# Performance work log

Hardware: AMD Instinct MI355X
Metric: run time of the kernel (lower is better)

The kernel has to match this reference:

```python
import jax, jax.numpy as jnp
import numpy as np

GROUP_SIZE = 64

def _dequant(wq, scale, zero):
    # HQQ groupwise dequant: W = (Wq - zero) * scale, groups along input dim.
    out_dim, in_dim = wq.shape
    g = in_dim // GROUP_SIZE
    w = (wq.astype(jnp.float32).reshape(out_dim, g, GROUP_SIZE) - zero[:, :, None]) * scale[:, :, None]
    return w.reshape(out_dim, in_dim)

def setup_inputs() -> dict:
    key = jax.random.key(0)
    ks = jax.random.split(key, 10)
    T, H, I = 256, 4096, 14336
    G1, G2 = H // GROUP_SIZE, I // GROUP_SIZE  # 64, 224
    x = jax.random.normal(ks[0], (T, H), dtype=jnp.float32)
    w1_q = jax.random.randint(ks[1], (I, H), 0, 16, dtype=jnp.int32)
    w1_scale = jax.random.uniform(ks[2], (I, G1), dtype=jnp.float32) * 0.02
    w1_zero = jax.random.uniform(ks[3], (I, G1), dtype=jnp.float32) * 8.0
    w3_q = jax.random.randint(ks[4], (I, H), 0, 16, dtype=jnp.int32)
    w3_scale = jax.random.uniform(ks[5], (I, G1), dtype=jnp.float32) * 0.02
    w3_zero = jax.random.uniform(ks[6], (I, G1), dtype=jnp.float32) * 8.0
    w2_q = jax.random.randint(ks[7], (H, I), 0, 16, dtype=jnp.int32)
    w2_scale = jax.random.uniform(ks[8], (H, G2), dtype=jnp.float32) * 0.02
    w2_zero = jax.random.uniform(ks[9], (H, G2), dtype=jnp.float32) * 8.0
    return {"x": x, "w1_q": w1_q, "w1_scale": w1_scale, "w1_zero": w1_zero,
            "w3_q": w3_q, "w3_scale": w3_scale, "w3_zero": w3_zero,
            "w2_q": w2_q, "w2_scale": w2_scale, "w2_zero": w2_zero}

def reference(x, w1_q, w1_scale, w1_zero, w3_q, w3_scale, w3_zero, w2_q, w2_scale, w2_zero):
    w1 = _dequant(w1_q, w1_scale, w1_zero)  # [I, H]
    w3 = _dequant(w3_q, w3_scale, w3_zero)  # [I, H]
    w2 = _dequant(w2_q, w2_scale, w2_zero)  # [H, I]
    gate = jax.nn.silu(jnp.einsum('th,ih->ti', x, w1))  # [T, I]
    up = jnp.einsum('th,ih->ti', x, w3)                 # [T, I]
    return jnp.einsum('ti,hi->th', gate * up, w2)       # [T, H]
```

## Files before the change

kernel.cpp:

```cpp
#include <hip/hip_runtime.h>
#include <cstdint>
#include <cstddef>

#define T_DIM 256
#define H_DIM 4096
#define I_DIM 14336

typedef __attribute__((ext_vector_type(8))) short s8v;
typedef __attribute__((ext_vector_type(4))) float f4v;

static constexpr size_t XS_BYTES   = (size_t)T_DIM * H_DIM * 2;
static constexpr size_t ACT_OFF    = XS_BYTES;
static constexpr size_t ACT_BYTES  = (size_t)T_DIM * I_DIM * 2;
static constexpr size_t PART_OFF   = ACT_OFF + ACT_BYTES;
static constexpr size_t PART_BYTES = 8ull * T_DIM * H_DIM * 4;
static constexpr size_t WS_NEEDED  = PART_OFF + PART_BYTES;

__device__ __forceinline__ unsigned short f2bf(float f) {
    unsigned u = __builtin_bit_cast(unsigned, f);
    u += 0x7fffu + ((u >> 16) & 1u);
    return (unsigned short)(u >> 16);
}

__device__ __forceinline__ void g2lds16(const void* g, void* l) {
    __builtin_amdgcn_global_load_lds(
        (const __attribute__((address_space(1))) unsigned int*)g,
        (__attribute__((address_space(3))) unsigned int*)l,
        16, 0, 0);
}

__device__ __forceinline__ s8v dq8(const int4 qa, const int4 qb, float s, float ns) {
    union { unsigned short u[8]; s8v v; } r;
    r.u[0] = f2bf(fmaf((float)qa.x, s, ns));
    r.u[1] = f2bf(fmaf((float)qa.y, s, ns));
    r.u[2] = f2bf(fmaf((float)qa.z, s, ns));
    r.u[3] = f2bf(fmaf((float)qa.w, s, ns));
    r.u[4] = f2bf(fmaf((float)qb.x, s, ns));
    r.u[5] = f2bf(fmaf((float)qb.y, s, ns));
    r.u[6] = f2bf(fmaf((float)qb.z, s, ns));
    r.u[7] = f2bf(fmaf((float)qb.w, s, ns));
    return r.v;
}

__global__ __launch_bounds__(256) void k_prep(const float* __restrict__ x,
                                              unsigned short* __restrict__ xs) {
    int gs   = blockIdx.x * 256 + threadIdx.x;
    int kt   = gs >> 11;
    int rem  = gs & 2047;
    int row  = rem >> 3;
    int slot = rem & 7;
    const float* xp = x + (size_t)row * H_DIM + kt * 64 + slot * 8;
    float4 a = *(const float4*)xp;
    float4 b = *(const float4*)(xp + 4);
    union { unsigned short u[8]; s8v v; } r;
    r.u[0] = f2bf(a.x); r.u[1] = f2bf(a.y); r.u[2] = f2bf(a.z); r.u[3] = f2bf(a.w);
    r.u[4] = f2bf(b.x); r.u[5] = f2bf(b.y); r.u[6] = f2bf(b.z); r.u[7] = f2bf(b.w);
    size_t di = (size_t)kt * 16384 + (size_t)row * 64 + (size_t)((slot ^ (row & 7)) * 8);
    *(s8v*)(xs + di) = r.v;
}

__global__ __launch_bounds__(512, 2) void k_gemm1(
    const int* __restrict__ w1q, const float* __restrict__ w1s, const float* __restrict__ w1z,
    const int* __restrict__ w3q, const float* __restrict__ w3s, const float* __restrict__ w3z,
    const unsigned short* __restrict__ xs, unsigned short* __restrict__ act)
{
    __shared__ unsigned char lds[49152];
    const int tid  = threadIdx.x;
    const int blk  = blockIdx.x;
    const int n0   = blk * 64;
    const int wid  = tid >> 6;
    const int lane = tid & 63;
    const int wr   = wid >> 1;
    const int wc   = wid & 1;
    const int lr   = lane & 15;
    const int lkb  = lane >> 4;
    const int aswz = (lr & 7) << 4;

    const int srow  = tid >> 3;
    const int sslot = tid & 7;
    const size_t grow = (size_t)(n0 + srow) * H_DIM + (size_t)sslot * 8;
    const int wbyte = srow * 128 + ((sslot * 16) ^ ((srow & 7) << 4));
    const float* s1p = w1s + (size_t)(n0 + srow) * 64;
    const float* z1p = w1z + (size_t)(n0 + srow) * 64;
    const float* s3p = w3s + (size_t)(n0 + srow) * 64;
    const float* z3p = w3z + (size_t)(n0 + srow) * 64;

    f4v accg[4][2], accu[4][2];
    const f4v fz = {0.f, 0.f, 0.f, 0.f};
    #pragma unroll
    for (int i = 0; i < 4; ++i)
        #pragma unroll
        for (int j = 0; j < 2; ++j) { accg[i][j] = fz; accu[i][j] = fz; }

    const unsigned char* xsb = (const unsigned char*)xs;

    for (int kt = 0; kt < 64; ++kt) {
        {
            const unsigned char* gsrc = xsb + (size_t)kt * 32768 + (size_t)wid * 1024
                                            + (size_t)lane * 16;
            unsigned char* ldst = lds + wid * 1024;
            #pragma unroll
            for (int j = 0; j < 4; ++j)
                g2lds16(gsrc + j * 8192, ldst + j * 8192);
        }
        {
            const int4* p1 = (const int4*)(w1q + grow + (size_t)kt * 64);
            const int4* p3 = (const int4*)(w3q + grow + (size_t)kt * 64);
            int4 q1a = p1[0], q1b = p1[1];
            int4 q3a = p3[0], q3b = p3[1];
            float s1 = s1p[kt]; float ns1 = -z1p[kt] * s1;
            float s3 = s3p[kt]; float ns3 = -z3p[kt] * s3;
            *(s8v*)(lds + 32768 + wbyte) = dq8(q1a, q1b, s1, ns1);
            *(s8v*)(lds + 40960 + wbyte) = dq8(q3a, q3b, s3, ns3);
        }
        __syncthreads();
        #pragma unroll
        for (int kf = 0; kf < 2; ++kf) {
            const int kb = (kf * 64 + lkb * 16) ^ aswz;
            s8v a[4];
            #pragma unroll
            for (int mf = 0; mf < 4; ++mf)
                a[mf] = *(const s8v*)(lds + (wr * 64 + mf * 16 + lr) * 128 + kb);
            s8v b1[2], b3[2];
            #pragma unroll
            for (int nf = 0; nf < 2; ++nf) {
                const int rbo = (wc * 32 + nf * 16 + lr) * 128 + kb;
                b1[nf] = *(const s8v*)(lds + 32768 + rbo);
                b3[nf] = *(const s8v*)(lds + 40960 + rbo);
            }
            #pragma unroll
            for (int mf = 0; mf < 4; ++mf)
                #pragma unroll
                for (int nf = 0; nf < 2; ++nf) {
                    accg[mf][nf] = __builtin_amdgcn_mfma_f32_16x16x32_bf16(a[mf], b1[nf], accg[mf][nf], 0, 0, 0);
                    accu[mf][nf] = __builtin_amdgcn_mfma_f32_16x16x32_bf16(a[mf], b3[nf], accu[mf][nf], 0, 0, 0);
                }
        }
        __syncthreads();
    }

    unsigned char* actb = (unsigned char*)act + (size_t)blk * 32768;
    #pragma unroll
    for (int mf = 0; mf < 4; ++mf)
        #pragma unroll
        for (int nf = 0; nf < 2; ++nf)
            #pragma unroll
            for (int r = 0; r < 4; ++r) {
                const int m  = wr * 64 + mf * 16 + lkb * 4 + r;
                const int nl = wc * 32 + nf * 16 + lr;
                float g = accg[mf][nf][r];
                float u = accu[mf][nf][r];
                float sg = g / (1.0f + __expf(-g));
                *(unsigned short*)(actb + ((m * 128 + nl * 2) ^ ((m & 7) << 4))) = f2bf(sg * u);
            }
}

template<bool ATOMIC>
__global__ __launch_bounds__(512, 2) void k_gemm2(
    const int* __restrict__ w2q, const float* __restrict__ w2s, const float* __restrict__ w2z,
    const unsigned short* __restrict__ act, float* __restrict__ outp)
{
    __shared__ unsigned char lds[49152];
    const int tid  = threadIdx.x;
    const int nb   = blockIdx.x & 31;
    const int kc   = blockIdx.x >> 5;
    const int n0   = nb * 128;
    const int wid  = tid >> 6;
    const int lane = tid & 63;
    const int wr   = wid >> 2;
    const int wc   = wid & 3;
    const int lr   = lane & 15;
    const int lkb  = lane >> 4;
    const int aswz = (lr & 7) << 4;

    const int srow = tid >> 2;
    const int ss2  = (tid & 3) * 2;
    const size_t grow = (size_t)(n0 + srow) * I_DIM + (size_t)ss2 * 8;
    const int wb0 = srow * 128 + ((ss2 * 16)       ^ ((srow & 7) << 4));
    const int wb1 = srow * 128 + (((ss2 + 1) * 16) ^ ((srow & 7) << 4));
    const float* s2p = w2s + (size_t)(n0 + srow) * 224;
    const float* z2p = w2z + (size_t)(n0 + srow) * 224;

    f4v acc[8][2];
    const f4v fz = {0.f, 0.f, 0.f, 0.f};
    #pragma unroll
    for (int i = 0; i < 8; ++i) { acc[i][0] = fz; acc[i][1] = fz; }

    const unsigned char* actb = (const unsigned char*)act;
    const int kt0 = kc * 28;

    for (int kk = 0; kk < 28; ++kk) {
        const int kt = kt0 + kk;
        {
            const unsigned char* gsrc = actb + (size_t)kt * 32768 + (size_t)wid * 1024
                                             + (size_t)lane * 16;
            unsigned char* ldst = lds + wid * 1024;
            #pragma unroll
            for (int j = 0; j < 4; ++j)
                g2lds16(gsrc + j * 8192, ldst + j * 8192);
        }
        {
            const int4* p2 = (const int4*)(w2q + grow + (size_t)kt * 64);
            int4 qa = p2[0], qb = p2[1], qc = p2[2], qd = p2[3];
            float s2 = s2p[kt]; float ns2 = -z2p[kt] * s2;
            *(s8v*)(lds + 32768 + wb0) = dq8(qa, qb, s2, ns2);
            *(s8v*)(lds + 32768 + wb1) = dq8(qc, qd, s2, ns2);
        }
        __syncthreads();
        #pragma unroll
        for (int kf = 0; kf < 2; ++kf) {
            const int kb = (kf * 64 + lkb * 16) ^ aswz;
            s8v b2[2];
            #pragma unroll
            for (int nf = 0; nf < 2; ++nf)
                b2[nf] = *(const s8v*)(lds + 32768 + (wc * 32 + nf * 16 + lr) * 128 + kb);
            #pragma unroll
            for (int mf = 0; mf < 8; ++mf) {
                s8v a = *(const s8v*)(lds + (wr * 128 + mf * 16 + lr) * 128 + kb);
                acc[mf][0] = __builtin_amdgcn_mfma_f32_16x16x32_bf16(a, b2[0], acc[mf][0], 0, 0, 0);
                acc[mf][1] = __builtin_amdgcn_mfma_f32_16x16x32_bf16(a, b2[1], acc[mf][1], 0, 0, 0);
            }
        }
        __syncthreads();
    }

    float* pout = outp + (ATOMIC ? 0 : (size_t)kc * ((size_t)T_DIM * H_DIM));
    #pragma unroll
    for (int mf = 0; mf < 8; ++mf)
        #pragma unroll
        for (int nf = 0; nf < 2; ++nf)
            #pragma unroll
            for (int r = 0; r < 4; ++r) {
                const int m = wr * 128 + mf * 16 + lkb * 4 + r;
                const int n = n0 + wc * 32 + nf * 16 + lr;
                if (ATOMIC) atomicAdd(&outp[(size_t)m * H_DIM + n], acc[mf][nf][r]);
                else        pout[(size_t)m * H_DIM + n] = acc[mf][nf][r];
            }
}

__global__ __launch_bounds__(256) void k_reduce(const f4v* __restrict__ p,
                                                f4v* __restrict__ o) {
    int i = blockIdx.x * 256 + threadIdx.x;
    f4v s = p[i];
    #pragma unroll
    for (int c = 1; c < 8; ++c) s += p[(size_t)c * 262144 + i];
    o[i] = s;
}

__global__ __launch_bounds__(256) void k_zero(f4v* __restrict__ o) {
    o[blockIdx.x * 256 + threadIdx.x] = (f4v){0.f, 0.f, 0.f, 0.f};
}

extern "C" void kernel_launch(void* const* d_in, const int* in_sizes, int n_in,
                              void* d_out, int out_size, void* d_ws, size_t ws_size,
                              hipStream_t stream) {
    const float* x   = (const float*)d_in[0];
    const int*   w1q = (const int*)  d_in[1];
    const float* w1s = (const float*)d_in[2];
    const float* w1z = (const float*)d_in[3];
    const int*   w3q = (const int*)  d_in[4];
    const float* w3s = (const float*)d_in[5];
    const float* w3z = (const float*)d_in[6];
    const int*   w2q = (const int*)  d_in[7];
    const float* w2s = (const float*)d_in[8];
    const float* w2z = (const float*)d_in[9];
    float* outp = (float*)d_out;

    unsigned short* xs  = (unsigned short*)d_ws;
    unsigned short* act = (unsigned short*)((char*)d_ws + ACT_OFF);
    float*          prt = (float*)((char*)d_ws + PART_OFF);
    const bool partials = (ws_size >= WS_NEEDED);

    k_prep<<<512, 256, 0, stream>>>(x, xs);
    k_gemm1<<<224, 512, 0, stream>>>(w1q, w1s, w1z, w3q, w3s, w3z, xs, act);
    if (partials) {
        k_gemm2<false><<<256, 512, 0, stream>>>(w2q, w2s, w2z, act, prt);
        k_reduce<<<1024, 256, 0, stream>>>((const f4v*)prt, (f4v*)outp);
    } else {
        k_zero<<<1024, 256, 0, stream>>>((f4v*)outp);
        k_gemm2<true><<<256, 512, 0, stream>>>(w2q, w2s, w2z, act, outp);
    }
}
```

Before: 284.9 us.

## Pack int4 weights, dequantize in registers into MFMA fragments, double-buffer activations

Adds a w_pack pass that repacks each weight tensor's 4-bit values, stored one per int32, into 8-per-dword words laid out in MFMA fragment order. Both GEMMs then dequantize directly in registers with packed bf16 conversion and skip the LDS staging of weights. Activations and x are pre-swizzled into fragment layout and double-buffered in LDS with prefetched weight loads, and GEMM2 is re-tiled to 64-column blocks with a 4-way K split. The packing pass still reads the full int32 weights every call, so the total weight traffic may grow rather than shrink unless packing is amortized.

After: 552.3 us. 1.94x slower.

```diff
diff --git a/kernel.cpp b/kernel.cpp
--- a/kernel.cpp
+++ b/kernel.cpp
@@ -9,12 +9,14 @@
 typedef __attribute__((ext_vector_type(8))) short s8v;
 typedef __attribute__((ext_vector_type(4))) float f4v;
 
-static constexpr size_t XS_BYTES   = (size_t)T_DIM * H_DIM * 2;
-static constexpr size_t ACT_OFF    = XS_BYTES;
-static constexpr size_t ACT_BYTES  = (size_t)T_DIM * I_DIM * 2;
-static constexpr size_t PART_OFF   = ACT_OFF + ACT_BYTES;
-static constexpr size_t PART_BYTES = 8ull * T_DIM * H_DIM * 4;
-static constexpr size_t WS_NEEDED  = PART_OFF + PART_BYTES;
+static constexpr size_t PRT_OFF   = 0;
+static constexpr size_t XS_OFF    = 16777216;
+static constexpr size_t ACT_OFF   = 18874368;
+static constexpr size_t P1_OFF    = 26214400;
+static constexpr size_t P3_OFF    = 55574528;
+static constexpr size_t P2_OFF    = 84934656;
+static constexpr size_t WS_PACKED = 114294784;
+static constexpr size_t WS_PART   = 26214400;
 
 __device__ __forceinline__ unsigned short f2bf(float f) {
     unsigned u = __builtin_bit_cast(unsigned, f);
@@ -29,61 +31,93 @@
         16, 0, 0);
 }
 
-__device__ __forceinline__ s8v dq8(const int4 qa, const int4 qb, float s, float ns) {
-    union { unsigned short u[8]; s8v v; } r;
-    r.u[0] = f2bf(fmaf((float)qa.x, s, ns));
-    r.u[1] = f2bf(fmaf((float)qa.y, s, ns));
-    r.u[2] = f2bf(fmaf((float)qa.z, s, ns));
-    r.u[3] = f2bf(fmaf((float)qa.w, s, ns));
-    r.u[4] = f2bf(fmaf((float)qb.x, s, ns));
-    r.u[5] = f2bf(fmaf((float)qb.y, s, ns));
-    r.u[6] = f2bf(fmaf((float)qb.z, s, ns));
-    r.u[7] = f2bf(fmaf((float)qb.w, s, ns));
-    return r.v;
+__device__ __forceinline__ s8v dqw(unsigned dw, float s, float ns) {
+    float f0 = fmaf((float)(dw & 15u), s, ns);
+    float f1 = fmaf((float)((dw >> 4) & 15u), s, ns);
+    float f2 = fmaf((float)((dw >> 8) & 15u), s, ns);
+    float f3 = fmaf((float)((dw >> 12) & 15u), s, ns);
+    float f4 = fmaf((float)((dw >> 16) & 15u), s, ns);
+    float f5 = fmaf((float)((dw >> 20) & 15u), s, ns);
+    float f6 = fmaf((float)((dw >> 24) & 15u), s, ns);
+    float f7 = fmaf((float)(dw >> 28), s, ns);
+    unsigned r0, r1, r2, r3;
+    asm("v_cvt_pk_bf16_f32 %0, %1, %2" : "=v"(r0) : "v"(f0), "v"(f1));
+    asm("v_cvt_pk_bf16_f32 %0, %1, %2" : "=v"(r1) : "v"(f2), "v"(f3));
+    asm("v_cvt_pk_bf16_f32 %0, %1, %2" : "=v"(r2) : "v"(f4), "v"(f5));
+    asm("v_cvt_pk_bf16_f32 %0, %1, %2" : "=v"(r3) : "v"(f6), "v"(f7));
+    union { unsigned u[4]; s8v v; } o;
+    o.u[0] = r0; o.u[1] = r1; o.u[2] = r2; o.u[3] = r3;
+    return o.v;
+}
+
+__device__ __forceinline__ s8v dq8f(const int4 qa, const int4 qb, float s, float ns) {
+    float f0 = fmaf((float)qa.x, s, ns), f1 = fmaf((float)qa.y, s, ns);
+    float f2 = fmaf((float)qa.z, s, ns), f3 = fmaf((float)qa.w, s, ns);
+    float f4 = fmaf((float)qb.x, s, ns), f5 = fmaf((float)qb.y, s, ns);
+    float f6 = fmaf((float)qb.z, s, ns), f7 = fmaf((float)qb.w, s, ns);
+    unsigned r0, r1, r2, r3;
+    asm("v_cvt_pk_bf16_f32 %0, %1, %2" : "=v"(r0) : "v"(f0), "v"(f1));
+    asm("v_cvt_pk_bf16_f32 %0, %1, %2" : "=v"(r1) : "v"(f2), "v"(f3));
+    asm("v_cvt_pk_bf16_f32 %0, %1, %2" : "=v"(r2) : "v"(f4), "v"(f5));
+    asm("v_cvt_pk_bf16_f32 %0, %1, %2" : "=v"(r3) : "v"(f6), "v"(f7));
+    union { unsigned u[4]; s8v v; } o;
+    o.u[0] = r0; o.u[1] = r1; o.u[2] = r2; o.u[3] = r3;
+    return o.v;
 }
 
 __global__ __launch_bounds__(256) void k_prep(const float* __restrict__ x,
                                               unsigned short* __restrict__ xs) {
-    int gs   = blockIdx.x * 256 + threadIdx.x;
-    int kt   = gs >> 11;
-    int rem  = gs & 2047;
-    int row  = rem >> 3;
-    int slot = rem & 7;
-    const float* xp = x + (size_t)row * H_DIM + kt * 64 + slot * 8;
+    int t = blockIdx.x * 256 + threadIdx.x;
+    int l = t & 63, f = t >> 6;
+    int msub = f & 15, ksub = f >> 4;
+    int m = msub * 16 + (l & 15);
+    int k = ksub * 32 + (l >> 4) * 8;
+    const float* xp = x + (size_t)m * H_DIM + k;
     float4 a = *(const float4*)xp;
     float4 b = *(const float4*)(xp + 4);
     union { unsigned short u[8]; s8v v; } r;
     r.u[0] = f2bf(a.x); r.u[1] = f2bf(a.y); r.u[2] = f2bf(a.z); r.u[3] = f2bf(a.w);
     r.u[4] = f2bf(b.x); r.u[5] = f2bf(b.y); r.u[6] = f2bf(b.z); r.u[7] = f2bf(b.w);
-    size_t di = (size_t)kt * 16384 + (size_t)row * 64 + (size_t)((slot ^ (row & 7)) * 8);
-    *(s8v*)(xs + di) = r.v;
-}
-
-__global__ __launch_bounds__(512, 2) void k_gemm1(
+    *((s8v*)xs + t) = r.v;
+}
+
+__global__ __launch_bounds__(256) void w_pack(const int* __restrict__ wq,
+                                              unsigned* __restrict__ p,
+                                              int K8, int bpr) {
+    int bx  = blockIdx.x;
+    int row = bx / bpr;
+    int oct = (bx - row * bpr) * 256 + threadIdx.x;
+    const int4* src = (const int4*)(wq + (size_t)row * (K8 * 8) + oct * 8);
+    int4 a = src[0], b = src[1];
+    unsigned dw = (unsigned)(a.x & 15) | ((unsigned)(a.y & 15) << 4)
+                | ((unsigned)(a.z & 15) << 8) | ((unsigned)(a.w & 15) << 12)
+                | ((unsigned)(b.x & 15) << 16) | ((unsigned)(b.y & 15) << 20)
+                | ((unsigned)(b.z & 15) << 24) | ((unsigned)(b.w & 15) << 28);
+    int nb = row >> 6, rl = row & 63, grp = rl >> 4;
+    int kt = oct >> 3, ks = (oct >> 2) & 1, lane = (rl & 15) + ((oct & 3) << 4);
+    p[(size_t)nb * (64 * (size_t)K8) + ((kt * 4 + grp) * 2 + ks) * 64 + lane] = dw;
+}
+
+struct Sc1 { float s1[2], z1[2], s3[2], z3[2]; };
+
+template<bool PACKED>
+__global__ __launch_bounds__(512) void k_gemm1(
     const int* __restrict__ w1q, const float* __restrict__ w1s, const float* __restrict__ w1z,
     const int* __restrict__ w3q, const float* __restrict__ w3s, const float* __restrict__ w3z,
-    const unsigned short* __restrict__ xs, unsigned short* __restrict__ act)
+    const unsigned* __restrict__ p1, const unsigned* __restrict__ p3,
+    const unsigned char* __restrict__ xs, unsigned char* __restrict__ act)
 {
-    __shared__ unsigned char lds[49152];
-    const int tid  = threadIdx.x;
-    const int blk  = blockIdx.x;
-    const int n0   = blk * 64;
-    const int wid  = tid >> 6;
-    const int lane = tid & 63;
-    const int wr   = wid >> 1;
-    const int wc   = wid & 1;
-    const int lr   = lane & 15;
-    const int lkb  = lane >> 4;
-    const int aswz = (lr & 7) << 4;
-
-    const int srow  = tid >> 3;
-    const int sslot = tid & 7;
-    const size_t grow = (size_t)(n0 + srow) * H_DIM + (size_t)sslot * 8;
-    const int wbyte = srow * 128 + ((sslot * 16) ^ ((srow & 7) << 4));
-    const float* s1p = w1s + (size_t)(n0 + srow) * 64;
-    const float* z1p = w1z + (size_t)(n0 + srow) * 64;
-    const float* s3p = w3s + (size_t)(n0 + srow) * 64;
-    const float* z3p = w3z + (size_t)(n0 + srow) * 64;
+    __shared__ unsigned char xbuf[2][32768];
+    const int tid = threadIdx.x, wid = tid >> 6, l = tid & 63;
+    const int lr = l & 15, lk = l >> 4;
+    const int wr = wid >> 1, wc = wid & 1;
+    const int nb = blockIdx.x, n0 = nb * 64;
+
+    const unsigned char* xsrc0 = xs + (size_t)(wid * 4) * 1024 + (size_t)l * 16;
+    const unsigned* p1b = p1 + (size_t)nb * 32768 + l;
+    const unsigned* p3b = p3 + (size_t)nb * 32768 + l;
+    const int row0 = n0 + wc * 32 + lr;
+    const int row1 = row0 + 16;
 
     f4v accg[4][2], accu[4][2];
     const f4v fz = {0.f, 0.f, 0.f, 0.f};
@@ -92,149 +126,196 @@
         #pragma unroll
         for (int j = 0; j < 2; ++j) { accg[i][j] = fz; accu[i][j] = fz; }
 
-    const unsigned char* xsb = (const unsigned char*)xs;
-
-    for (int kt = 0; kt < 64; ++kt) {
-        {
-            const unsigned char* gsrc = xsb + (size_t)kt * 32768 + (size_t)wid * 1024
-                                            + (size_t)lane * 16;
-            unsigned char* ldst = lds + wid * 1024;
-            #pragma unroll
-            for (int j = 0; j < 4; ++j)
-                g2lds16(gsrc + j * 8192, ldst + j * 8192);
-        }
-        {
-            const int4* p1 = (const int4*)(w1q + grow + (size_t)kt * 64);
-            const int4* p3 = (const int4*)(w3q + grow + (size_t)kt * 64);
-            int4 q1a = p1[0], q1b = p1[1];
-            int4 q3a = p3[0], q3b = p3[1];
-            float s1 = s1p[kt]; float ns1 = -z1p[kt] * s1;
-            float s3 = s3p[kt]; float ns3 = -z3p[kt] * s3;
-            *(s8v*)(lds + 32768 + wbyte) = dq8(q1a, q1b, s1, ns1);
-            *(s8v*)(lds + 40960 + wbyte) = dq8(q3a, q3b, s3, ns3);
-        }
+    unsigned Dp1[2][4], Dp3[2][4];
+    int4 Qa1[2][4], Qb1[2][4], Qa3[2][4], Qb3[2][4];
+    Sc1 S[2];
+
+    auto stage = [&](int t) {
+        unsigned char* dst = xbuf[t & 1] + (size_t)(wid * 4) * 1024;
+        const unsigned char* src = xsrc0 + (size_t)t * 32768;
+        #pragma unroll
+        for (int j = 0; j < 4; ++j)
+            g2lds16(src + j * 1024, dst + j * 1024);
+    };
+    auto wload = [&](int kt, int slot) {
+        #pragma unroll
+        for (int nf = 0; nf < 2; ++nf) {
+            const int row = nf ? row1 : row0;
+            S[slot].s1[nf] = w1s[(size_t)row * 64 + kt];
+            S[slot].z1[nf] = w1z[(size_t)row * 64 + kt];
+            S[slot].s3[nf] = w3s[(size_t)row * 64 + kt];
+            S[slot].z3[nf] = w3z[(size_t)row * 64 + kt];
+            #pragma unroll
+            for (int ks = 0; ks < 2; ++ks) {
+                if constexpr (PACKED) {
+                    const int off = ((kt * 4 + wc * 2 + nf) * 2 + ks) * 64;
+                    Dp1[slot][nf * 2 + ks] = p1b[off];
+                    Dp3[slot][nf * 2 + ks] = p3b[off];
+                } else {
+                    const int4* q1 = (const int4*)(w1q + (size_t)row * H_DIM + kt * 64 + ks * 32 + lk * 8);
+                    const int4* q3 = (const int4*)(w3q + (size_t)row * H_DIM + kt * 64 + ks * 32 + lk * 8);
+                    Qa1[slot][nf * 2 + ks] = q1[0]; Qb1[slot][nf * 2 + ks] = q1[1];
+                    Qa3[slot][nf * 2 + ks] = q3[0]; Qb3[slot][nf * 2 + ks] = q3[1];
+                }
+            }
+        }
+    };
+    auto compute = [&](int t, int slot) {
+        const unsigned char* xb = xbuf[t & 1];
+        #pragma unroll
+        for (int ks = 0; ks < 2; ++ks) {
+            s8v a[4];
+            #pragma unroll
+            for (int mf = 0; mf < 4; ++mf)
+                a[mf] = *(const s8v*)(xb + (ks * 16 + wr * 4 + mf) * 1024 + l * 16);
+            #pragma unroll
+            for (int nf = 0; nf < 2; ++nf) {
+                const float ss1 = S[slot].s1[nf], nz1 = -S[slot].z1[nf] * ss1;
+                const float ss3 = S[slot].s3[nf], nz3 = -S[slot].z3[nf] * ss3;
+                s8v B1, B3;
+                if constexpr (PACKED) {
+                    B1 = dqw(Dp1[slot][nf * 2 + ks], ss1, nz1);
+                    B3 = dqw(Dp3[slot][nf * 2 + ks], ss3, nz3);
+                } else {
+                    B1 = dq8f(Qa1[slot][nf * 2 + ks], Qb1[slot][nf * 2 + ks], ss1, nz1);
+                    B3 = dq8f(Qa3[slot][nf * 2 + ks], Qb3[slot][nf * 2 + ks], ss3, nz3);
+                }
+                #pragma unroll
+                for (int mf = 0; mf < 4; ++mf) {
+                    accg[mf][nf] = __builtin_amdgcn_mfma_f32_16x16x32_bf16(a[mf], B1, accg[mf][nf], 0, 0, 0);
+                    accu[mf][nf] = __builtin_amdgcn_mfma_f32_16x16x32_bf16(a[mf], B3, accu[mf][nf], 0, 0, 0);
+                }
+            }
+        }
+    };
+
+    stage(0); wload(0, 0);
+    __syncthreads();
+    for (int i = 0; i < 32; ++i) {
+        const int t = i * 2;
+        if (t + 1 < 64) { stage(t + 1); wload(t + 1, 1); }
+        compute(t, 0);
         __syncthreads();
-        #pragma unroll
-        for (int kf = 0; kf < 2; ++kf) {
-            const int kb = (kf * 64 + lkb * 16) ^ aswz;
-            s8v a[4];
-            #pragma unroll
-            for (int mf = 0; mf < 4; ++mf)
-                a[mf] = *(const s8v*)(lds + (wr * 64 + mf * 16 + lr) * 128 + kb);
-            s8v b1[2], b3[2];
-            #pragma unroll
-            for (int nf = 0; nf < 2; ++nf) {
-                const int rbo = (wc * 32 + nf * 16 + lr) * 128 + kb;
-                b1[nf] = *(const s8v*)(lds + 32768 + rbo);
-                b3[nf] = *(const s8v*)(lds + 40960 + rbo);
-            }
-            #pragma unroll
-            for (int mf = 0; mf < 4; ++mf)
-                #pragma unroll
-                for (int nf = 0; nf < 2; ++nf) {
-                    accg[mf][nf] = __builtin_amdgcn_mfma_f32_16x16x32_bf16(a[mf], b1[nf], accg[mf][nf], 0, 0, 0);
-                    accu[mf][nf] = __builtin_amdgcn_mfma_f32_16x16x32_bf16(a[mf], b3[nf], accu[mf][nf], 0, 0, 0);
-                }
-        }
+        if (t + 2 < 64) { stage(t + 2); wload(t + 2, 0); }
+        compute(t + 1, 1);
         __syncthreads();
     }
 
-    unsigned char* actb = (unsigned char*)act + (size_t)blk * 32768;
+    unsigned char* ab = act + (size_t)nb * 32768;
     #pragma unroll
     for (int mf = 0; mf < 4; ++mf)
         #pragma unroll
         for (int nf = 0; nf < 2; ++nf)
             #pragma unroll
             for (int r = 0; r < 4; ++r) {
-                const int m  = wr * 64 + mf * 16 + lkb * 4 + r;
-                const int nl = wc * 32 + nf * 16 + lr;
-                float g = accg[mf][nf][r];
-                float u = accu[mf][nf][r];
+                float g = accg[mf][nf][r], u = accu[mf][nf][r];
                 float sg = g / (1.0f + __expf(-g));
-                *(unsigned short*)(actb + ((m * 128 + nl * 2) ^ ((m & 7) << 4))) = f2bf(sg * u);
-            }
-}
-
-template<bool ATOMIC>
-__global__ __launch_bounds__(512, 2) void k_gemm2(
+                const int F     = wc * 16 + wr * 4 + mf;
+                const int lane2 = (lk * 4 + r) + 16 * (nf * 2 + (lr >> 3));
+                *(unsigned short*)(ab + F * 1024 + lane2 * 16 + (lr & 7) * 2) = f2bf(sg * u);
+            }
+}
+
+struct Sc2 { float s[2], z[2]; };
+
+template<bool PACKED, bool ATOMIC>
+__global__ __launch_bounds__(512) void k_gemm2(
     const int* __restrict__ w2q, const float* __restrict__ w2s, const float* __restrict__ w2z,
-    const unsigned short* __restrict__ act, float* __restrict__ outp)
+    const unsigned* __restrict__ p2,
+    const unsigned char* __restrict__ act, float* __restrict__ outp)
 {
-    __shared__ unsigned char lds[49152];
-    const int tid  = threadIdx.x;
-    const int nb   = blockIdx.x & 31;
-    const int kc   = blockIdx.x >> 5;
-    const int n0   = nb * 128;
-    const int wid  = tid >> 6;
-    const int lane = tid & 63;
-    const int wr   = wid >> 2;
-    const int wc   = wid & 3;
-    const int lr   = lane & 15;
-    const int lkb  = lane >> 4;
-    const int aswz = (lr & 7) << 4;
-
-    const int srow = tid >> 2;
-    const int ss2  = (tid & 3) * 2;
-    const size_t grow = (size_t)(n0 + srow) * I_DIM + (size_t)ss2 * 8;
-    const int wb0 = srow * 128 + ((ss2 * 16)       ^ ((srow & 7) << 4));
-    const int wb1 = srow * 128 + (((ss2 + 1) * 16) ^ ((srow & 7) << 4));
-    const float* s2p = w2s + (size_t)(n0 + srow) * 224;
-    const float* z2p = w2z + (size_t)(n0 + srow) * 224;
-
-    f4v acc[8][2];
+    __shared__ unsigned char xbuf[2][32768];
+    const int tid = threadIdx.x, wid = tid >> 6, l = tid & 63;
+    const int lr = l & 15, lk = l >> 4;
+    const int wr = wid >> 1, wc = wid & 1;
+    const int bx = blockIdx.x;
+    const int kc = (bx & 7) >> 1;
+    const int nb = (bx >> 3) * 2 + (bx & 1);
+    const int n0 = nb * 64;
+    const int T0 = kc * 56;
+
+    const unsigned char* asrc0 = act + (size_t)(wid * 4) * 1024 + (size_t)l * 16;
+    const unsigned* p2b = p2 + (size_t)nb * 114688 + l;
+    const int row0 = n0 + wc * 32 + lr;
+    const int row1 = row0 + 16;
+
+    f4v acc[4][2];
     const f4v fz = {0.f, 0.f, 0.f, 0.f};
     #pragma unroll
-    for (int i = 0; i < 8; ++i) { acc[i][0] = fz; acc[i][1] = fz; }
-
-    const unsigned char* actb = (const unsigned char*)act;
-    const int kt0 = kc * 28;
-
-    for (int kk = 0; kk < 28; ++kk) {
-        const int kt = kt0 + kk;
-        {
-            const unsigned char* gsrc = actb + (size_t)kt * 32768 + (size_t)wid * 1024
-                                             + (size_t)lane * 16;
-            unsigned char* ldst = lds + wid * 1024;
-            #pragma unroll
-            for (int j = 0; j < 4; ++j)
-                g2lds16(gsrc + j * 8192, ldst + j * 8192);
-        }
-        {
-            const int4* p2 = (const int4*)(w2q + grow + (size_t)kt * 64);
-            int4 qa = p2[0], qb = p2[1], qc = p2[2], qd = p2[3];
-            float s2 = s2p[kt]; float ns2 = -z2p[kt] * s2;
-            *(s8v*)(lds + 32768 + wb0) = dq8(qa, qb, s2, ns2);
-            *(s8v*)(lds + 32768 + wb1) = dq8(qc, qd, s2, ns2);
-        }
+    for (int i = 0; i < 4; ++i) { acc[i][0] = fz; acc[i][1] = fz; }
+
+    unsigned Dp[2][4];
+    int4 Qa[2][4], Qb[2][4];
+    Sc2 S[2];
+
+    auto stage = [&](int t) {
+        unsigned char* dst = xbuf[t & 1] + (size_t)(wid * 4) * 1024;
+        const unsigned char* src = asrc0 + (size_t)(T0 + t) * 32768;
+        #pragma unroll
+        for (int j = 0; j < 4; ++j)
+            g2lds16(src + j * 1024, dst + j * 1024);
+    };
+    auto wload = [&](int t, int slot) {
+        const int kt = T0 + t;
+        #pragma unroll
+        for (int nf = 0; nf < 2; ++nf) {
+            const int row = nf ? row1 : row0;
+            S[slot].s[nf] = w2s[(size_t)row * 224 + kt];
+            S[slot].z[nf] = w2z[(size_t)row * 224 + kt];
+            #pragma unroll
+            for (int ks = 0; ks < 2; ++ks) {
+                if constexpr (PACKED) {
+                    Dp[slot][nf * 2 + ks] = p2b[((kt * 4 + wc * 2 + nf) * 2 + ks) * 64];
+                } else {
+                    const int4* q = (const int4*)(w2q + (size_t)row * I_DIM + kt * 64 + ks * 32 + lk * 8);
+                    Qa[slot][nf * 2 + ks] = q[0]; Qb[slot][nf * 2 + ks] = q[1];
+                }
+            }
+        }
+    };
+    auto compute = [&](int t, int slot) {
+        const unsigned char* xb = xbuf[t & 1];
+        #pragma unroll
+        for (int ks = 0; ks < 2; ++ks) {
+            s8v a[4];
+            #pragma unroll
+            for (int mf = 0; mf < 4; ++mf)
+                a[mf] = *(const s8v*)(xb + (ks * 16 + wr * 4 + mf) * 1024 + l * 16);
+            #pragma unroll
+            for (int nf = 0; nf < 2; ++nf) {
+                const float ss = S[slot].s[nf], nz = -S[slot].z[nf] * ss;
+                s8v B = PACKED ? dqw(Dp[slot][nf * 2 + ks], ss, nz)
+                               : dq8f(Qa[slot][nf * 2 + ks], Qb[slot][nf * 2 + ks], ss, nz);
+                #pragma unroll
+                for (int mf = 0; mf < 4; ++mf)
+                    acc[mf][nf] = __builtin_amdgcn_mfma_f32_16x16x32_bf16(a[mf], B, acc[mf][nf], 0, 0, 0);
+            }
+        }
+    };
+
+    stage(0); wload(0, 0);
+    __syncthreads();
+    for (int i = 0; i < 28; ++i) {
+        const int t = i * 2;
+        if (t + 1 < 56) { stage(t + 1); wload(t + 1, 1); }
+        compute(t, 0);
         __syncthreads();
-        #pragma unroll
-        for (int kf = 0; kf < 2; ++kf) {
-            const int kb = (kf * 64 + lkb * 16) ^ aswz;
-            s8v b2[2];
-            #pragma unroll
-            for (int nf = 0; nf < 2; ++nf)
-                b2[nf] = *(const s8v*)(lds + 32768 + (wc * 32 + nf * 16 + lr) * 128 + kb);
-            #pragma unroll
-            for (int mf = 0; mf < 8; ++mf) {
-                s8v a = *(const s8v*)(lds + (wr * 128 + mf * 16 + lr) * 128 + kb);
-                acc[mf][0] = __builtin_amdgcn_mfma_f32_16x16x32_bf16(a, b2[0], acc[mf][0], 0, 0, 0);
-                acc[mf][1] = __builtin_amdgcn_mfma_f32_16x16x32_bf16(a, b2[1], acc[mf][1], 0, 0, 0);
-            }
-        }
+        if (t + 2 < 56) { stage(t + 2); wload(t + 2, 0); }
+        compute(t + 1, 1);
         __syncthreads();
     }
 
     float* pout = outp + (ATOMIC ? 0 : (size_t)kc * ((size_t)T_DIM * H_DIM));
     #pragma unroll
-    for (int mf = 0; mf < 8; ++mf)
+    for (int mf = 0; mf < 4; ++mf)
         #pragma unroll
         for (int nf = 0; nf < 2; ++nf)
             #pragma unroll
             for (int r = 0; r < 4; ++r) {
-                const int m = wr * 128 + mf * 16 + lkb * 4 + r;
-                const int n = n0 + wc * 32 + nf * 16 + lr;
-                if (ATOMIC) atomicAdd(&outp[(size_t)m * H_DIM + n], acc[mf][nf][r]);
-                else        pout[(size_t)m * H_DIM + n] = acc[mf][nf][r];
+                const int M = wr * 64 + mf * 16 + lk * 4 + r;
+                const int N = n0 + wc * 32 + nf * 16 + lr;
+                if (ATOMIC) atomicAdd(&outp[(size_t)M * H_DIM + N], acc[mf][nf][r]);
+                else        pout[(size_t)M * H_DIM + N] = acc[mf][nf][r];
             }
 }
 
@@ -243,7 +324,7 @@
     int i = blockIdx.x * 256 + threadIdx.x;
     f4v s = p[i];
     #pragma unroll
-    for (int c = 1; c < 8; ++c) s += p[(size_t)c * 262144 + i];
+    for (int c = 1; c < 4; ++c) s += p[(size_t)c * 262144 + i];
     o[i] = s;
 }
 
@@ -266,18 +347,34 @@
     const float* w2z = (const float*)d_in[9];
     float* outp = (float*)d_out;
 
-    unsigned short* xs  = (unsigned short*)d_ws;
-    unsigned short* act = (unsigned short*)((char*)d_ws + ACT_OFF);
-    float*          prt = (float*)((char*)d_ws + PART_OFF);
-    const bool partials = (ws_size >= WS_NEEDED);
+    const bool big    = (ws_size >= WS_PART);
+    const bool packed = (ws_size >= WS_PACKED);
+
+    unsigned short* xs  = (unsigned short*)((char*)d_ws + (big ? XS_OFF : 0));
+    unsigned char*  act = (unsigned char*)d_ws + (big ? ACT_OFF : 2097152);
+    float*    prt = (float*)d_ws;
+    unsigned* p1  = (unsigned*)((char*)d_ws + P1_OFF);
+    unsigned* p3  = (unsigned*)((char*)d_ws + P3_OFF);
+    unsigned* p2  = (unsigned*)((char*)d_ws + P2_OFF);
 
     k_prep<<<512, 256, 0, stream>>>(x, xs);
-    k_gemm1<<<224, 512, 0, stream>>>(w1q, w1s, w1z, w3q, w3s, w3z, xs, act);
-    if (partials) {
-        k_gemm2<false><<<256, 512, 0, stream>>>(w2q, w2s, w2z, act, prt);
+    if (packed) {
+        w_pack<<<28672, 256, 0, stream>>>(w1q, p1, 512, 2);
+        w_pack<<<28672, 256, 0, stream>>>(w3q, p3, 512, 2);
+        w_pack<<<28672, 256, 0, stream>>>(w2q, p2, 1792, 7);
+        k_gemm1<true><<<224, 512, 0, stream>>>(w1q, w1s, w1z, w3q, w3s, w3z,
+                                               p1, p3, (const unsigned char*)xs, act);
+        k_gemm2<true, false><<<256, 512, 0, stream>>>(w2q, w2s, w2z, p2, act, prt);
         k_reduce<<<1024, 256, 0, stream>>>((const f4v*)prt, (f4v*)outp);
     } else {
-        k_zero<<<1024, 256, 0, stream>>>((f4v*)outp);
-        k_gemm2<true><<<256, 512, 0, stream>>>(w2q, w2s, w2z, act, outp);
+        k_gemm1<false><<<224, 512, 0, stream>>>(w1q, w1s, w1z, w3q, w3s, w3z,
+                                                p1, p3, (const unsigned char*)xs, act);
+        if (big) {
+            k_gemm2<false, false><<<256, 512, 0, stream>>>(w2q, w2s, w2z, p2, act, prt);
+            k_reduce<<<1024, 256, 0, stream>>>((const f4v*)prt, (f4v*)outp);
+        } else {
+            k_zero<<<1024, 256, 0, stream>>>((f4v*)outp);
+            k_gemm2<false, true><<<256, 512, 0, stream>>>(w2q, w2s, w2z, p2, act, outp);
+        }
     }
 }
```
